# Kernel tuning notes

Measured on AMD Instinct MI355X. Metric: run time of the kernel, lower is better.

The kernel has to match this reference:

```python
import jax, jax.numpy as jnp
import numpy as np
import math

EPS = 1e-6

def _rmsnorm(x, w):
    var = jnp.mean(x * x, axis=-1, keepdims=True)
    return x * jax.lax.rsqrt(var + EPS) * w

def _rotary(x, cos, sin):
    d = x.shape[-1] // 2
    x1, x2 = x[..., :d], x[..., d:]
    return jnp.concatenate([x1 * cos - x2 * sin, x2 * cos + x1 * sin], axis=-1)

def _conv1x1(x, w):
    # x: (B, C, 1, S), w: (O, C) -> (B, O, 1, S)
    return jnp.einsum('bcls,oc->bols', x, w)

def setup_inputs() -> dict:
    key = jax.random.key(0)
    ks = jax.random.split(key, 12)
    B, H, KVH, D, S, T, HID = 8, 16, 2, 128, 16, 8192, 2048
    return {
        'x': jax.random.normal(ks[0], (B, HID, 1, S), jnp.float32),
        'cos': jax.random.uniform(ks[1], (1, 1, S, D // 2), jnp.float32),
        'sin': jax.random.uniform(ks[2], (1, 1, S, D // 2), jnp.float32),
        'kv_cache_k': jax.random.normal(ks[3], (B, KVH, T, D), jnp.float32),
        'kv_cache_v': jax.random.normal(ks[4], (B, KVH, T, D), jnp.float32),
        'position': 4096,
        'mask': jnp.zeros((1, 1, S, T), jnp.float32),
        'wq': jax.random.normal(ks[5], (H * D, HID), jnp.float32) * 0.02,
        'wk': jax.random.normal(ks[6], (KVH * D, HID), jnp.float32) * 0.02,
        'wv': jax.random.normal(ks[7], (KVH * D, HID), jnp.float32) * 0.02,
        'wo': jax.random.normal(ks[8], (HID, H * D), jnp.float32) * 0.02,
        'q_norm_w': jnp.ones((D,), jnp.float32),
        'k_norm_w': jnp.ones((D,), jnp.float32),
    }

def reference(x, cos, sin, kv_cache_k, kv_cache_v, position, mask,
              wq, wk, wv, wo, q_norm_w, k_norm_w):
    B, S = x.shape[0], x.shape[3]
    D = q_norm_w.shape[0]
    H = wq.shape[0] // D
    KVH = wk.shape[0] // D
    G = H // KVH  # GQA group size

    # projections (1x1 conv == channel matmul), then (B, h, S, D)
    q = _conv1x1(x, wq)[:, :, 0, :].reshape(B, H, D, S).transpose(0, 1, 3, 2)
    k = _conv1x1(x, wk)[:, :, 0, :].reshape(B, KVH, D, S).transpose(0, 1, 3, 2)
    v = _conv1x1(x, wv)[:, :, 0, :].reshape(B, KVH, D, S).transpose(0, 1, 3, 2)

    q = _rotary(_rmsnorm(q, q_norm_w), cos, sin)
    k = _rotary(_rmsnorm(k, k_norm_w), cos, sin)

    # scatter new k/v into cache at `position`
    new_k = jax.lax.dynamic_update_slice(kv_cache_k, k, (0, 0, position, 0))
    new_v = jax.lax.dynamic_update_slice(kv_cache_v, v, (0, 0, position, 0))

    # GQA: fold q heads into (kv_head, group) so K/V need no repeat_interleave
    scale = 1.0 / math.sqrt(D)
    qg = q.reshape(B, KVH, G, S, D)
    attn = jnp.einsum('bkgsd,bktd->bkgst', qg, new_k) * scale
    attn = attn + mask[:, :, None, :, :]  # (1,1,S,T) -> broadcast over groups
    probs = jax.nn.softmax(attn, axis=-1)
    out = jnp.einsum('bkgst,bktd->bkgsd', probs, new_v).reshape(B, H, S, D)

    # back to (B, H*D, 1, S) and output projection
    out = out.transpose(0, 1, 3, 2).reshape(B, H * D, 1, S)
    out = _conv1x1(out, wo)
    return out, new_k, new_v
```

## Files before the change

### kernel.cpp

```cpp
#include <hip/hip_runtime.h>
#include <cstdint>
#include <cstddef>


typedef __attribute__((ext_vector_type(8))) short bf16x8;
typedef __attribute__((ext_vector_type(4))) float f32x4;
typedef unsigned short u16;
typedef unsigned int u32;

#define MFMA16(a, b, c) __builtin_amdgcn_mfma_f32_16x16x32_bf16(a, b, c, 0, 0, 0)

static __device__ __forceinline__ u16 f2bf(float f) {
  u32 u = __float_as_uint(f);
  u += 0x7FFFu + ((u >> 16) & 1u);
  return (u16)(u >> 16);
}
static __device__ __forceinline__ float bf2f(u16 u) {
  return __uint_as_float(((u32)u) << 16);
}
static __device__ __forceinline__ u32 pk2(float a, float b) {
  return (u32)f2bf(a) | ((u32)f2bf(b) << 16);
}

__global__ __launch_bounds__(256) void transpose_x(const float* __restrict__ x,
                                                   u16* __restrict__ Xt) {
  int id = blockIdx.x * 256 + threadIdx.x;
  int b = id >> 13, c = (id >> 2) & 2047, s4 = id & 3;
  float4 v = *(const float4*)(x + ((size_t)(b * 2048 + c)) * 16 + s4 * 4);
  size_t base = (size_t)(b * 16 + s4 * 4) * 2048 + c;
  Xt[base]        = f2bf(v.x);
  Xt[base + 2048] = f2bf(v.y);
  Xt[base + 4096] = f2bf(v.z);
  Xt[base + 6144] = f2bf(v.w);
}

template <int MODE>
__global__ __launch_bounds__(256) void gemm16(const float* __restrict__ w0,
                                              const float* __restrict__ w1,
                                              const float* __restrict__ w2,
                                              const u16* __restrict__ Bt,
                                              float* __restrict__ outp) {
  __shared__ __align__(16) u16 sW[16 * 256];
  const int tid = threadIdx.x, lane = tid & 63, w = tid >> 6;
  const int q = lane >> 4, n = lane & 15;
  const int m0 = blockIdx.x * 16;
  const float* wbase;
  if (MODE == 0) {
    if (m0 < 2048)      wbase = w0 + (size_t)m0 * 2048;
    else if (m0 < 2304) wbase = w1 + (size_t)(m0 - 2048) * 2048;
    else                wbase = w2 + (size_t)(m0 - 2304) * 2048;
  } else {
    wbase = w0 + (size_t)m0 * 2048;
  }
  f32x4 acc0 = {0.f, 0.f, 0.f, 0.f}, acc1 = acc0;

  for (int c0 = 0; c0 < 2048; c0 += 256) {
    {
      int m = tid >> 4, s16 = tid & 15;
      const float* src = wbase + (size_t)m * 2048 + c0 + s16 * 16;
      float4 a = *(const float4*)(src);
      float4 b = *(const float4*)(src + 4);
      float4 c = *(const float4*)(src + 8);
      float4 d = *(const float4*)(src + 12);
      uint4 u0 = {pk2(a.x, a.y), pk2(a.z, a.w), pk2(b.x, b.y), pk2(b.z, b.w)};
      uint4 u1 = {pk2(c.x, c.y), pk2(c.z, c.w), pk2(d.x, d.y), pk2(d.z, d.w)};
      int G0 = 2 * s16;
      *(uint4*)&sW[m * 256 + ((G0 + m) & 31) * 8]     = u0;
      *(uint4*)&sW[m * 256 + ((G0 + 1 + m) & 31) * 8] = u1;
    }
    __syncthreads();
    bf16x8 bfr[2][8];
#pragma unroll
    for (int e = 0; e < 2; ++e) {
      int j = 32 * w + 16 * e + n;
      const u16* bp = Bt + (size_t)j * 2048 + c0 + q * 8;
#pragma unroll
      for (int ks = 0; ks < 8; ++ks) bfr[e][ks] = *(const bf16x8*)(bp + ks * 32);
    }
#pragma unroll
    for (int ks = 0; ks < 8; ++ks) {
      bf16x8 af = *(const bf16x8*)&sW[n * 256 + (((4 * ks + q) + n) & 31) * 8];
      acc0 = MFMA16(af, bfr[0][ks], acc0);
      acc1 = MFMA16(af, bfr[1][ks], acc1);
    }
    __syncthreads();
  }
#pragma unroll
  for (int e = 0; e < 2; ++e) {
    f32x4 a = e ? acc1 : acc0;
    int j = 32 * w + 16 * e + n;
#pragma unroll
    for (int reg = 0; reg < 4; ++reg) {
      int m = m0 + 4 * q + reg;
      if (MODE == 0) outp[(size_t)m * 128 + j] = a[reg];
      else outp[(size_t)(j >> 4) * 32768 + m * 16 + (j & 15)] = a[reg];
    }
  }
}

__global__ __launch_bounds__(256) void norm_rot(
    const float* __restrict__ qkv, const float* __restrict__ cosb,
    const float* __restrict__ sinb, const float* __restrict__ qw,
    const float* __restrict__ kw,
    u16* __restrict__ Qa, float* __restrict__ knew, float* __restrict__ vnew) {
  const int wid = blockIdx.x * 4 + (threadIdx.x >> 6);
  const int lane = threadIdx.x & 63;
  const float SCALE = 0.08838834764831845f;
  if (wid < 2048) {
    int b = wid >> 8, h = (wid >> 4) & 15, s = wid & 15;
    int j = b * 16 + s;
    float v1 = qkv[(size_t)(h * 128 + lane) * 128 + j];
    float v2 = qkv[(size_t)(h * 128 + lane + 64) * 128 + j];
    float ss = v1 * v1 + v2 * v2;
#pragma unroll
    for (int o = 32; o > 0; o >>= 1) ss += __shfl_xor(ss, o, 64);
    float rr = rsqrtf(ss * (1.0f / 128.0f) + 1e-6f);
    float n1 = v1 * rr * qw[lane];
    float n2 = v2 * rr * qw[lane + 64];
    float c = cosb[s * 64 + lane], sn = sinb[s * 64 + lane];
    u16* dst = Qa + (size_t)((b * 16 + h) * 16 + s) * 128;
    dst[lane]      = f2bf((n1 * c - n2 * sn) * SCALE);
    dst[lane + 64] = f2bf((n2 * c + n1 * sn) * SCALE);
  } else if (wid < 2304) {
    int idx = wid - 2048;
    int b = idx >> 5, kvh = (idx >> 4) & 1, s = idx & 15;
    int j = b * 16 + s;
    int row = 2048 + kvh * 128;
    float v1 = qkv[(size_t)(row + lane) * 128 + j];
    float v2 = qkv[(size_t)(row + lane + 64) * 128 + j];
    float ss = v1 * v1 + v2 * v2;
#pragma unroll
    for (int o = 32; o > 0; o >>= 1) ss += __shfl_xor(ss, o, 64);
    float rr = rsqrtf(ss * (1.0f / 128.0f) + 1e-6f);
    float n1 = v1 * rr * kw[lane];
    float n2 = v2 * rr * kw[lane + 64];
    float c = cosb[s * 64 + lane], sn = sinb[s * 64 + lane];
    float* dst = knew + (size_t)((b * 2 + kvh) * 16 + s) * 128;
    dst[lane]      = n1 * c - n2 * sn;
    dst[lane + 64] = n2 * c + n1 * sn;
  } else {
    int idx = wid - 2304;
    int b = idx >> 5, kvh = (idx >> 4) & 1, s = idx & 15;
    int j = b * 16 + s;
    int row = 2304 + kvh * 128;
    float* dst = vnew + (size_t)((b * 2 + kvh) * 16 + s) * 128;
    dst[lane]      = qkv[(size_t)(row + lane) * 128 + j];
    dst[lane + 64] = qkv[(size_t)(row + lane + 64) * 128 + j];
  }
}

__global__ __launch_bounds__(256, 2) void attn(
    const u16* __restrict__ Qa, const float* __restrict__ kcache,
    const float* __restrict__ vcache, const float* __restrict__ knew,
    const float* __restrict__ vnew, const int* __restrict__ posp,
    const float* __restrict__ mask, float* __restrict__ outk,
    float* __restrict__ outv, u16* __restrict__ Opart,
    float* __restrict__ Mpart, float* __restrict__ Lpart) {
  __shared__ __align__(16) u16 sQ[16384];
  __shared__ __align__(16) u16 sP[8192];
  __shared__ __align__(16) u16 sVt[8192];

  const int tid = threadIdx.x, lane = tid & 63, w = tid >> 6;
  const int q = lane >> 4, n = lane & 15;
  const int bid = blockIdx.x;
  const int bk = bid >> 5, chunk = bid & 31;
  const int b = bk >> 1, kvh = bk & 1;
  const int pos = *posp;

  for (int i = tid; i < 2048; i += 256) {
    int r = i >> 4, g = i & 15;
    int h = kvh * 8 + (r >> 4), s = r & 15;
    uint4 v = *(const uint4*)(Qa + (size_t)((b * 16 + h) * 16 + s) * 128 + g * 8);
    *(uint4*)&sQ[r * 128 + ((g + r) & 15) * 8] = v;
  }
  __syncthreads();
  bf16x8 qf[2][4];
#pragma unroll
  for (int e = 0; e < 2; ++e) {
    int r = 32 * w + 16 * e + n;
#pragma unroll
    for (int ks = 0; ks < 4; ++ks)
      qf[e][ks] = *(const bf16x8*)&sQ[r * 128 + (((4 * ks + q) + r) & 15) * 8];
  }
  __syncthreads();

  bf16x8 idE = {0, 0, 0, 0, 0, 0, 0, 0}, idO = idE;
  {
    const short one = (short)0x3F80;
    int tq = n >> 3, te = n & 7;
#pragma unroll
    for (int e = 0; e < 8; ++e) {
      if (q == tq && e == te) idE[e] = one;
      if (q == tq + 2 && e == te) idO[e] = one;
    }
  }

  float m_old[2] = {-INFINITY, -INFINITY}, l_old[2] = {0.f, 0.f};
  f32x4 oacc[2][8];
#pragma unroll
  for (int e = 0; e < 2; ++e)
#pragma unroll
    for (int nt = 0; nt < 8; ++nt) oacc[e][nt] = (f32x4){0.f, 0.f, 0.f, 0.f};

  for (int tile = 0; tile < 4; ++tile) {
    const int t0 = chunk * 256 + tile * 64;
    for (int i = tid; i < 2048; i += 256) {
      int isV = i >> 10;
      int tl = (i >> 4) & 63, g = i & 15;
      int tg = t0 + tl;
      const float* src;
      float* dst;
      if (!isV) {
        src = (tg >= pos && tg < pos + 16)
                  ? (knew + (size_t)(bk * 16 + (tg - pos)) * 128)
                  : (kcache + ((size_t)bk * 8192 + tg) * 128);
        dst = outk + ((size_t)bk * 8192 + tg) * 128;
      } else {
        src = (tg >= pos && tg < pos + 16)
                  ? (vnew + (size_t)(bk * 16 + (tg - pos)) * 128)
                  : (vcache + ((size_t)bk * 8192 + tg) * 128);
        dst = outv + ((size_t)bk * 8192 + tg) * 128;
      }
      float4 a = *(const float4*)(src + g * 8);
      float4 b2 = *(const float4*)(src + g * 8 + 4);
      *(float4*)(dst + g * 8) = a;
      *(float4*)(dst + g * 8 + 4) = b2;
      uint4 u = {pk2(a.x, a.y), pk2(a.z, a.w), pk2(b2.x, b2.y), pk2(b2.z, b2.w)};
      *(uint4*)&sQ[isV * 8192 + tl * 128 + ((g + tl) & 15) * 8] = u;
    }
    float mv[4][4];
#pragma unroll
    for (int mt = 0; mt < 4; ++mt)
#pragma unroll
      for (int rg = 0; rg < 4; ++rg)
        mv[mt][rg] = mask[(size_t)n * 8192 + t0 + 16 * mt + 4 * q + rg];
    __syncthreads();

    f32x4 sacc[4][2];
#pragma unroll
    for (int mt = 0; mt < 4; ++mt) {
      sacc[mt][0] = (f32x4){0.f, 0.f, 0.f, 0.f};
      sacc[mt][1] = sacc[mt][0];
    }
#pragma unroll
    for (int ks = 0; ks < 4; ++ks) {
#pragma unroll
      for (int mt = 0; mt < 4; ++mt) {
        int trow = 16 * mt + n;
        bf16x8 kf = *(const bf16x8*)&sQ[trow * 128 + (((4 * ks + q) + trow) & 15) * 8];
        sacc[mt][0] = MFMA16(kf, qf[0][ks], sacc[mt][0]);
        sacc[mt][1] = MFMA16(kf, qf[1][ks], sacc[mt][1]);
      }
    }

#pragma unroll
    for (int mtv = 0; mtv < 4; ++mtv) {
      int trow = 16 * mtv + n;
      bf16x8 vfr = *(const bf16x8*)&sQ[8192 + trow * 128 + (((4 * w + q) + trow) & 15) * 8];
      f32x4 z = {0.f, 0.f, 0.f, 0.f};
      f32x4 d0 = MFMA16(vfr, idE, z);
      f32x4 d1 = MFMA16(vfr, idO, z);
      int G = 2 * mtv + (q >> 1), off = 4 * (q & 1);
      int dp0 = 32 * w + n, dp1 = dp0 + 16;
      uint2 u0 = {pk2(d0[0], d0[1]), pk2(d0[2], d0[3])};
      uint2 u1 = {pk2(d1[0], d1[1]), pk2(d1[2], d1[3])};
      *(uint2*)&sVt[dp0 * 64 + ((G + dp0) & 7) * 8 + off] = u0;
      *(uint2*)&sVt[dp1 * 64 + ((G + dp1) & 7) * 8 + off] = u1;
    }

    float al[2];
#pragma unroll
    for (int e = 0; e < 2; ++e) {
      float sv[4][4];
      float mx = -INFINITY;
#pragma unroll
      for (int mt = 0; mt < 4; ++mt)
#pragma unroll
        for (int rg = 0; rg < 4; ++rg) {
          float v = sacc[mt][e][rg] + mv[mt][rg];
          sv[mt][rg] = v;
          mx = fmaxf(mx, v);
        }
      mx = fmaxf(mx, __shfl_xor(mx, 16));
      mx = fmaxf(mx, __shfl_xor(mx, 32));
      float mn = fmaxf(m_old[e], mx);
      al[e] = __expf(m_old[e] - mn);
      float ts = 0.f;
      int r = 32 * w + 16 * e + n;
#pragma unroll
      for (int mt = 0; mt < 4; ++mt) {
        float p0 = __expf(sv[mt][0] - mn), p1 = __expf(sv[mt][1] - mn);
        float p2 = __expf(sv[mt][2] - mn), p3 = __expf(sv[mt][3] - mn);
        ts += (p0 + p1) + (p2 + p3);
        uint2 up = {pk2(p0, p1), pk2(p2, p3)};
        int G = 2 * mt + (q >> 1), off = 4 * (q & 1);
        *(uint2*)&sP[r * 64 + ((G + r) & 7) * 8 + off] = up;
      }
      ts += __shfl_xor(ts, 16);
      ts += __shfl_xor(ts, 32);
      l_old[e] = l_old[e] * al[e] + ts;
      m_old[e] = mn;
    }
    __syncthreads();

#pragma unroll
    for (int e = 0; e < 2; ++e) {
      float an[4];
#pragma unroll
      for (int rg = 0; rg < 4; ++rg) an[rg] = __shfl(al[e], 4 * q + rg);
#pragma unroll
      for (int nt = 0; nt < 8; ++nt)
#pragma unroll
        for (int rg = 0; rg < 4; ++rg) oacc[e][nt][rg] *= an[rg];
    }
    bf16x8 Pf[2][2];
#pragma unroll
    for (int e = 0; e < 2; ++e) {
      int r = 32 * w + 16 * e + n;
#pragma unroll
      for (int ks = 0; ks < 2; ++ks)
        Pf[e][ks] = *(const bf16x8*)&sP[r * 64 + (((4 * ks + q) + r) & 7) * 8];
    }
#pragma unroll
    for (int nt = 0; nt < 8; ++nt) {
      int d = 16 * nt + n;
#pragma unroll
      for (int ks = 0; ks < 2; ++ks) {
        bf16x8 vf = *(const bf16x8*)&sVt[d * 64 + (((4 * ks + q) + d) & 7) * 8];
        oacc[0][nt] = MFMA16(Pf[0][ks], vf, oacc[0][nt]);
        oacc[1][nt] = MFMA16(Pf[1][ks], vf, oacc[1][nt]);
      }
    }
    __syncthreads();
  }

#pragma unroll
  for (int e = 0; e < 2; ++e)
#pragma unroll
    for (int nt = 0; nt < 8; ++nt) {
      int d = 16 * nt + n;
      int r0 = 32 * w + 16 * e + 4 * q;
      int G = r0 >> 3, off = 4 * (q & 1);
      uint2 u = {pk2(oacc[e][nt][0], oacc[e][nt][1]),
                 pk2(oacc[e][nt][2], oacc[e][nt][3])};
      *(uint2*)&sQ[d * 128 + ((G + d) & 15) * 8 + off] = u;
    }
  if (q == 0) {
#pragma unroll
    for (int e = 0; e < 2; ++e) {
      int r = 32 * w + 16 * e + n;
      Mpart[(size_t)bid * 128 + r] = m_old[e];
      Lpart[(size_t)bid * 128 + r] = l_old[e];
    }
  }
  __syncthreads();
  for (int i = tid; i < 2048; i += 256) {
    int d = i >> 4, g = i & 15;
    uint4 v = *(const uint4*)&sQ[d * 128 + ((g + d) & 15) * 8];
    *(uint4*)(Opart + (size_t)bid * 16384 + d * 128 + g * 8) = v;
  }
}

__global__ __launch_bounds__(256) void combine(const u16* __restrict__ Opart,
                                               const float* __restrict__ Mp,
                                               const float* __restrict__ Lp,
                                               u16* __restrict__ A2t) {
  __shared__ float wgt[32 * 128];
  const int tid = threadIdx.x;
  const int bk = blockIdx.x, dgrp = blockIdx.y;
  if (tid < 128) {
    int r = tid;
    float mc[32], M = -INFINITY;
#pragma unroll
    for (int c = 0; c < 32; ++c) {
      mc[c] = Mp[(size_t)(bk * 32 + c) * 128 + r];
      M = fmaxf(M, mc[c]);
    }
    float L = 0.f, wv[32];
#pragma unroll
    for (int c = 0; c < 32; ++c) {
      wv[c] = __expf(mc[c] - M);
      L += wv[c] * Lp[(size_t)(bk * 32 + c) * 128 + r];
    }
    float inv = 1.0f / L;
#pragma unroll
    for (int c = 0; c < 32; ++c) wgt[c * 128 + r] = wv[c] * inv;
  }
  __syncthreads();
  int r = tid & 127, dd = tid >> 7;
  int b = bk >> 1, kvh = bk & 1;
  int h = kvh * 8 + (r >> 4), s = r & 15;
  size_t arow = (size_t)(b * 16 + s) * 2048 + h * 128;
  for (int di = 0; di < 8; ++di) {
    int d = dgrp * 16 + dd + 2 * di;
    float o = 0.f;
#pragma unroll
    for (int c = 0; c < 32; ++c)
      o += wgt[c * 128 + r] *
           bf2f(Opart[((size_t)(bk * 32 + c) * 128 + d) * 128 + r]);
    A2t[arow + d] = f2bf(o);
  }
}

extern "C" void kernel_launch(void* const* d_in, const int* in_sizes, int n_in,
                              void* d_out, int out_size, void* d_ws, size_t ws_size,
                              hipStream_t stream) {
  const float* x    = (const float*)d_in[0];
  const float* cosb = (const float*)d_in[1];
  const float* sinb = (const float*)d_in[2];
  const float* kc   = (const float*)d_in[3];
  const float* vc   = (const float*)d_in[4];
  const int*   posp = (const int*)d_in[5];
  const float* mask = (const float*)d_in[6];
  const float* wq   = (const float*)d_in[7];
  const float* wk   = (const float*)d_in[8];
  const float* wv   = (const float*)d_in[9];
  const float* wo   = (const float*)d_in[10];
  const float* qw   = (const float*)d_in[11];
  const float* kw   = (const float*)d_in[12];

  float* out  = (float*)d_out;
  float* outk = out + 262144;
  float* outv = outk + 16777216;

  float* ws      = (float*)d_ws;
  float* ws_qkv  = ws;
  float* ws_knew = ws + 327680;
  float* ws_vnew = ws + 360448;
  u16*   ws_Qa   = (u16*)(ws + 393216);
  u16*   ws_Xt   = (u16*)(ws + 524288);
  u16*   ws_A2t  = (u16*)(ws + 655360);
  float* ws_M    = ws + 786432;
  float* ws_L    = ws + 851968;
  u16*   ws_O    = (u16*)(ws + 917504);

  transpose_x<<<256, 256, 0, stream>>>(x, ws_Xt);
  gemm16<0><<<160, 256, 0, stream>>>(wq, wk, wv, ws_Xt, ws_qkv);
  norm_rot<<<640, 256, 0, stream>>>(ws_qkv, cosb, sinb, qw, kw,
                                    ws_Qa, ws_knew, ws_vnew);
  attn<<<512, 256, 0, stream>>>(ws_Qa, kc, vc, ws_knew, ws_vnew, posp, mask,
                                outk, outv, ws_O, ws_M, ws_L);
  combine<<<dim3(16, 8), 256, 0, stream>>>(ws_O, ws_M, ws_L, ws_A2t);
  gemm16<1><<<128, 256, 0, stream>>>(wo, wo, wo, ws_A2t, out);
}
```

Measured before the change: 346.3 us.

## Prefetch KV tiles in registers, split-K GEMM blocks, transpose QKV output layout

The attention kernel now loads the next K/V tile into registers while the current tile is being computed, and it prefetches the mask. Q fragments are read straight from global memory instead of being staged through LDS. One of the per-tile barriers is dropped by merging the LDS buffers into one region. The projection GEMMs use 512-thread blocks that split K across two halves and reduce through LDS. The QKV output is stored row-major per token, so the GEMM writes and the norm_rot reads are contiguous. In exchange, register pressure in the attention kernel rises, and removing the trailing barrier needs the LDS regions to be disjoint to stay race-free.

After: 365.9 us. 1.06x slower.

```diff
diff --git a/kernel.cpp b/kernel.cpp
--- a/kernel.cpp
+++ b/kernel.cpp
@@ -35,13 +35,17 @@
 }
 
 template <int MODE>
-__global__ __launch_bounds__(256) void gemm16(const float* __restrict__ w0,
+__global__ __launch_bounds__(512) void gemm16(const float* __restrict__ w0,
                                               const float* __restrict__ w1,
                                               const float* __restrict__ w2,
                                               const u16* __restrict__ Bt,
                                               float* __restrict__ outp) {
-  __shared__ __align__(16) u16 sW[16 * 256];
-  const int tid = threadIdx.x, lane = tid & 63, w = tid >> 6;
+  __shared__ __align__(16) u16 sW[2][16 * 256];
+  __shared__ __align__(16) float sRed[2048];
+  const int t512 = threadIdx.x;
+  const int half = t512 >> 8;
+  const int tid = t512 & 255;
+  const int lane = tid & 63, w = tid >> 6;
   const int q = lane >> 4, n = lane & 15;
   const int m0 = blockIdx.x * 16;
   const float* wbase;
@@ -52,9 +56,10 @@
   } else {
     wbase = w0 + (size_t)m0 * 2048;
   }
+  const int kbase = half * 1024;
   f32x4 acc0 = {0.f, 0.f, 0.f, 0.f}, acc1 = acc0;
 
-  for (int c0 = 0; c0 < 2048; c0 += 256) {
+  for (int c0 = kbase; c0 < kbase + 1024; c0 += 256) {
     {
       int m = tid >> 4, s16 = tid & 15;
       const float* src = wbase + (size_t)m * 2048 + c0 + s16 * 16;
@@ -65,8 +70,8 @@
       uint4 u0 = {pk2(a.x, a.y), pk2(a.z, a.w), pk2(b.x, b.y), pk2(b.z, b.w)};
       uint4 u1 = {pk2(c.x, c.y), pk2(c.z, c.w), pk2(d.x, d.y), pk2(d.z, d.w)};
       int G0 = 2 * s16;
-      *(uint4*)&sW[m * 256 + ((G0 + m) & 31) * 8]     = u0;
-      *(uint4*)&sW[m * 256 + ((G0 + 1 + m) & 31) * 8] = u1;
+      *(uint4*)&sW[half][m * 256 + ((G0 + m) & 31) * 8]     = u0;
+      *(uint4*)&sW[half][m * 256 + ((G0 + 1 + m) & 31) * 8] = u1;
     }
     __syncthreads();
     bf16x8 bfr[2][8];
@@ -79,21 +84,33 @@
     }
 #pragma unroll
     for (int ks = 0; ks < 8; ++ks) {
-      bf16x8 af = *(const bf16x8*)&sW[n * 256 + (((4 * ks + q) + n) & 31) * 8];
+      bf16x8 af = *(const bf16x8*)&sW[half][n * 256 + (((4 * ks + q) + n) & 31) * 8];
       acc0 = MFMA16(af, bfr[0][ks], acc0);
       acc1 = MFMA16(af, bfr[1][ks], acc1);
     }
     __syncthreads();
   }
-#pragma unroll
-  for (int e = 0; e < 2; ++e) {
-    f32x4 a = e ? acc1 : acc0;
-    int j = 32 * w + 16 * e + n;
-#pragma unroll
-    for (int reg = 0; reg < 4; ++reg) {
-      int m = m0 + 4 * q + reg;
-      if (MODE == 0) outp[(size_t)m * 128 + j] = a[reg];
-      else outp[(size_t)(j >> 4) * 32768 + m * 16 + (j & 15)] = a[reg];
+  if (half == 1) {
+    *(f32x4*)&sRed[tid * 8]     = acc0;
+    *(f32x4*)&sRed[tid * 8 + 4] = acc1;
+  }
+  __syncthreads();
+  if (half == 0) {
+    acc0 += *(const f32x4*)&sRed[tid * 8];
+    acc1 += *(const f32x4*)&sRed[tid * 8 + 4];
+#pragma unroll
+    for (int e = 0; e < 2; ++e) {
+      f32x4 a = e ? acc1 : acc0;
+      int j = 32 * w + 16 * e + n;
+      if (MODE == 0) {
+        *(f32x4*)&outp[(size_t)j * 2560 + m0 + 4 * q] = a;
+      } else {
+#pragma unroll
+        for (int reg = 0; reg < 4; ++reg) {
+          int m = m0 + 4 * q + reg;
+          outp[(size_t)(j >> 4) * 32768 + m * 16 + (j & 15)] = a[reg];
+        }
+      }
     }
   }
 }
@@ -109,8 +126,9 @@
   if (wid < 2048) {
     int b = wid >> 8, h = (wid >> 4) & 15, s = wid & 15;
     int j = b * 16 + s;
-    float v1 = qkv[(size_t)(h * 128 + lane) * 128 + j];
-    float v2 = qkv[(size_t)(h * 128 + lane + 64) * 128 + j];
+    const float* row = qkv + (size_t)j * 2560 + h * 128;
+    float v1 = row[lane];
+    float v2 = row[lane + 64];
     float ss = v1 * v1 + v2 * v2;
 #pragma unroll
     for (int o = 32; o > 0; o >>= 1) ss += __shfl_xor(ss, o, 64);
@@ -125,9 +143,9 @@
     int idx = wid - 2048;
     int b = idx >> 5, kvh = (idx >> 4) & 1, s = idx & 15;
     int j = b * 16 + s;
-    int row = 2048 + kvh * 128;
-    float v1 = qkv[(size_t)(row + lane) * 128 + j];
-    float v2 = qkv[(size_t)(row + lane + 64) * 128 + j];
+    const float* row = qkv + (size_t)j * 2560 + 2048 + kvh * 128;
+    float v1 = row[lane];
+    float v2 = row[lane + 64];
     float ss = v1 * v1 + v2 * v2;
 #pragma unroll
     for (int o = 32; o > 0; o >>= 1) ss += __shfl_xor(ss, o, 64);
@@ -142,10 +160,10 @@
     int idx = wid - 2304;
     int b = idx >> 5, kvh = (idx >> 4) & 1, s = idx & 15;
     int j = b * 16 + s;
-    int row = 2304 + kvh * 128;
+    const float* row = qkv + (size_t)j * 2560 + 2304 + kvh * 128;
     float* dst = vnew + (size_t)((b * 2 + kvh) * 16 + s) * 128;
-    dst[lane]      = qkv[(size_t)(row + lane) * 128 + j];
-    dst[lane + 64] = qkv[(size_t)(row + lane + 64) * 128 + j];
+    dst[lane]      = row[lane];
+    dst[lane + 64] = row[lane + 64];
   }
 }
 
@@ -156,9 +174,7 @@
     const float* __restrict__ mask, float* __restrict__ outk,
     float* __restrict__ outv, u16* __restrict__ Opart,
     float* __restrict__ Mpart, float* __restrict__ Lpart) {
-  __shared__ __align__(16) u16 sQ[16384];
-  __shared__ __align__(16) u16 sP[8192];
-  __shared__ __align__(16) u16 sVt[8192];
+  __shared__ __align__(16) u16 lds[32768];
 
   const int tid = threadIdx.x, lane = tid & 63, w = tid >> 6;
   const int q = lane >> 4, n = lane & 15;
@@ -167,22 +183,54 @@
   const int b = bk >> 1, kvh = bk & 1;
   const int pos = *posp;
 
-  for (int i = tid; i < 2048; i += 256) {
-    int r = i >> 4, g = i & 15;
-    int h = kvh * 8 + (r >> 4), s = r & 15;
-    uint4 v = *(const uint4*)(Qa + (size_t)((b * 16 + h) * 16 + s) * 128 + g * 8);
-    *(uint4*)&sQ[r * 128 + ((g + r) & 15) * 8] = v;
-  }
-  __syncthreads();
+  const int stl = tid >> 4;
+  const int g = tid & 15;
+
+#define SRC_PTR(isV_, tg_)                                                   \
+  ((isV_) ? (((tg_) >= pos && (tg_) < pos + 16)                              \
+                 ? (vnew + (size_t)(bk * 16 + ((tg_) - pos)) * 128)          \
+                 : (vcache + ((size_t)bk * 8192 + (tg_)) * 128))             \
+          : (((tg_) >= pos && (tg_) < pos + 16)                              \
+                 ? (knew + (size_t)(bk * 16 + ((tg_) - pos)) * 128)          \
+                 : (kcache + ((size_t)bk * 8192 + (tg_)) * 128)))
+
+  float4 pf[8][2];
+#define ISSUE_STAGE(tile_)                                                   \
+  {                                                                          \
+    const int t0_ = chunk * 256 + (tile_) * 64;                              \
+    _Pragma("unroll") for (int u = 0; u < 8; ++u) {                          \
+      int isV_ = u >> 2;                                                     \
+      int tl_ = (stl + 16 * u) & 63;                                         \
+      int tg_ = t0_ + tl_;                                                   \
+      const float* s_ = SRC_PTR(isV_, tg_) + g * 8;                          \
+      pf[u][0] = *(const float4*)(s_);                                       \
+      pf[u][1] = *(const float4*)(s_ + 4);                                   \
+    }                                                                        \
+  }
+
+  float4 mv4[4];
+#define LOAD_MASK(tile_)                                                     \
+  {                                                                          \
+    const int t0_ = chunk * 256 + (tile_) * 64;                              \
+    _Pragma("unroll") for (int mt = 0; mt < 4; ++mt)                         \
+        mv4[mt] =                                                            \
+        *(const float4*)(mask + (size_t)n * 8192 + t0_ + 16 * mt + 4 * q);   \
+  }
+
+  ISSUE_STAGE(0);
+
   bf16x8 qf[2][4];
 #pragma unroll
   for (int e = 0; e < 2; ++e) {
     int r = 32 * w + 16 * e + n;
+    int h = kvh * 8 + (r >> 4), s = r & 15;
+    const u16* qrow = Qa + (size_t)((b * 16 + h) * 16 + s) * 128;
 #pragma unroll
     for (int ks = 0; ks < 4; ++ks)
-      qf[e][ks] = *(const bf16x8*)&sQ[r * 128 + (((4 * ks + q) + r) & 15) * 8];
-  }
-  __syncthreads();
+      qf[e][ks] = *(const bf16x8*)(qrow + (4 * ks + q) * 8);
+  }
+
+  LOAD_MASK(0);
 
   bf16x8 idE = {0, 0, 0, 0, 0, 0, 0, 0}, idO = idE;
   {
@@ -204,37 +252,21 @@
 
   for (int tile = 0; tile < 4; ++tile) {
     const int t0 = chunk * 256 + tile * 64;
-    for (int i = tid; i < 2048; i += 256) {
-      int isV = i >> 10;
-      int tl = (i >> 4) & 63, g = i & 15;
+#pragma unroll
+    for (int u = 0; u < 8; ++u) {
+      int isV = u >> 2;
+      int tl = (stl + 16 * u) & 63;
       int tg = t0 + tl;
-      const float* src;
-      float* dst;
-      if (!isV) {
-        src = (tg >= pos && tg < pos + 16)
-                  ? (knew + (size_t)(bk * 16 + (tg - pos)) * 128)
-                  : (kcache + ((size_t)bk * 8192 + tg) * 128);
-        dst = outk + ((size_t)bk * 8192 + tg) * 128;
-      } else {
-        src = (tg >= pos && tg < pos + 16)
-                  ? (vnew + (size_t)(bk * 16 + (tg - pos)) * 128)
-                  : (vcache + ((size_t)bk * 8192 + tg) * 128);
-        dst = outv + ((size_t)bk * 8192 + tg) * 128;
-      }
-      float4 a = *(const float4*)(src + g * 8);
-      float4 b2 = *(const float4*)(src + g * 8 + 4);
-      *(float4*)(dst + g * 8) = a;
-      *(float4*)(dst + g * 8 + 4) = b2;
-      uint4 u = {pk2(a.x, a.y), pk2(a.z, a.w), pk2(b2.x, b2.y), pk2(b2.z, b2.w)};
-      *(uint4*)&sQ[isV * 8192 + tl * 128 + ((g + tl) & 15) * 8] = u;
-    }
-    float mv[4][4];
-#pragma unroll
-    for (int mt = 0; mt < 4; ++mt)
-#pragma unroll
-      for (int rg = 0; rg < 4; ++rg)
-        mv[mt][rg] = mask[(size_t)n * 8192 + t0 + 16 * mt + 4 * q + rg];
+      float* dst = (isV ? outv : outk) + ((size_t)bk * 8192 + tg) * 128 + g * 8;
+      float4 a = pf[u][0], b2 = pf[u][1];
+      *(float4*)dst = a;
+      *(float4*)(dst + 4) = b2;
+      uint4 uu = {pk2(a.x, a.y), pk2(a.z, a.w), pk2(b2.x, b2.y), pk2(b2.z, b2.w)};
+      *(uint4*)&lds[isV * 8192 + tl * 128 + ((g + tl) & 15) * 8] = uu;
+    }
     __syncthreads();
+
+    if (tile < 3) { ISSUE_STAGE(tile + 1); }
 
     f32x4 sacc[4][2];
 #pragma unroll
@@ -247,7 +279,7 @@
 #pragma unroll
       for (int mt = 0; mt < 4; ++mt) {
         int trow = 16 * mt + n;
-        bf16x8 kf = *(const bf16x8*)&sQ[trow * 128 + (((4 * ks + q) + trow) & 15) * 8];
+        bf16x8 kf = *(const bf16x8*)&lds[trow * 128 + (((4 * ks + q) + trow) & 15) * 8];
         sacc[mt][0] = MFMA16(kf, qf[0][ks], sacc[mt][0]);
         sacc[mt][1] = MFMA16(kf, qf[1][ks], sacc[mt][1]);
       }
@@ -256,7 +288,7 @@
 #pragma unroll
     for (int mtv = 0; mtv < 4; ++mtv) {
       int trow = 16 * mtv + n;
-      bf16x8 vfr = *(const bf16x8*)&sQ[8192 + trow * 128 + (((4 * w + q) + trow) & 15) * 8];
+      bf16x8 vfr = *(const bf16x8*)&lds[8192 + trow * 128 + (((4 * w + q) + trow) & 15) * 8];
       f32x4 z = {0.f, 0.f, 0.f, 0.f};
       f32x4 d0 = MFMA16(vfr, idE, z);
       f32x4 d1 = MFMA16(vfr, idO, z);
@@ -264,8 +296,8 @@
       int dp0 = 32 * w + n, dp1 = dp0 + 16;
       uint2 u0 = {pk2(d0[0], d0[1]), pk2(d0[2], d0[3])};
       uint2 u1 = {pk2(d1[0], d1[1]), pk2(d1[2], d1[3])};
-      *(uint2*)&sVt[dp0 * 64 + ((G + dp0) & 7) * 8 + off] = u0;
-      *(uint2*)&sVt[dp1 * 64 + ((G + dp1) & 7) * 8 + off] = u1;
+      *(uint2*)&lds[24576 + dp0 * 64 + ((G + dp0) & 7) * 8 + off] = u0;
+      *(uint2*)&lds[24576 + dp1 * 64 + ((G + dp1) & 7) * 8 + off] = u1;
     }
 
     float al[2];
@@ -277,7 +309,7 @@
       for (int mt = 0; mt < 4; ++mt)
 #pragma unroll
         for (int rg = 0; rg < 4; ++rg) {
-          float v = sacc[mt][e][rg] + mv[mt][rg];
+          float v = sacc[mt][e][rg] + mv4[mt][rg];
           sv[mt][rg] = v;
           mx = fmaxf(mx, v);
         }
@@ -294,13 +326,14 @@
         ts += (p0 + p1) + (p2 + p3);
         uint2 up = {pk2(p0, p1), pk2(p2, p3)};
         int G = 2 * mt + (q >> 1), off = 4 * (q & 1);
-        *(uint2*)&sP[r * 64 + ((G + r) & 7) * 8 + off] = up;
+        *(uint2*)&lds[16384 + r * 64 + ((G + r) & 7) * 8 + off] = up;
       }
       ts += __shfl_xor(ts, 16);
       ts += __shfl_xor(ts, 32);
       l_old[e] = l_old[e] * al[e] + ts;
       m_old[e] = mn;
     }
+    if (tile < 3) { LOAD_MASK(tile + 1); }
     __syncthreads();
 
 #pragma unroll
@@ -319,19 +352,18 @@
       int r = 32 * w + 16 * e + n;
 #pragma unroll
       for (int ks = 0; ks < 2; ++ks)
-        Pf[e][ks] = *(const bf16x8*)&sP[r * 64 + (((4 * ks + q) + r) & 7) * 8];
+        Pf[e][ks] = *(const bf16x8*)&lds[16384 + r * 64 + (((4 * ks + q) + r) & 7) * 8];
     }
 #pragma unroll
     for (int nt = 0; nt < 8; ++nt) {
       int d = 16 * nt + n;
 #pragma unroll
       for (int ks = 0; ks < 2; ++ks) {
-        bf16x8 vf = *(const bf16x8*)&sVt[d * 64 + (((4 * ks + q) + d) & 7) * 8];
+        bf16x8 vf = *(const bf16x8*)&lds[24576 + d * 64 + (((4 * ks + q) + d) & 7) * 8];
         oacc[0][nt] = MFMA16(Pf[0][ks], vf, oacc[0][nt]);
         oacc[1][nt] = MFMA16(Pf[1][ks], vf, oacc[1][nt]);
       }
     }
-    __syncthreads();
   }
 
 #pragma unroll
@@ -343,7 +375,7 @@
       int G = r0 >> 3, off = 4 * (q & 1);
       uint2 u = {pk2(oacc[e][nt][0], oacc[e][nt][1]),
                  pk2(oacc[e][nt][2], oacc[e][nt][3])};
-      *(uint2*)&sQ[d * 128 + ((G + d) & 15) * 8 + off] = u;
+      *(uint2*)&lds[d * 128 + ((G + d) & 15) * 8 + off] = u;
     }
   if (q == 0) {
 #pragma unroll
@@ -355,10 +387,13 @@
   }
   __syncthreads();
   for (int i = tid; i < 2048; i += 256) {
-    int d = i >> 4, g = i & 15;
-    uint4 v = *(const uint4*)&sQ[d * 128 + ((g + d) & 15) * 8];
-    *(uint4*)(Opart + (size_t)bid * 16384 + d * 128 + g * 8) = v;
-  }
+    int d2 = i >> 4, g2 = i & 15;
+    uint4 v = *(const uint4*)&lds[d2 * 128 + ((g2 + d2) & 15) * 8];
+    *(uint4*)(Opart + (size_t)bid * 16384 + d2 * 128 + g2 * 8) = v;
+  }
+#undef SRC_PTR
+#undef ISSUE_STAGE
+#undef LOAD_MASK
 }
 
 __global__ __launch_bounds__(256) void combine(const u16* __restrict__ Opart,
@@ -435,11 +470,11 @@
   u16*   ws_O    = (u16*)(ws + 917504);
 
   transpose_x<<<256, 256, 0, stream>>>(x, ws_Xt);
-  gemm16<0><<<160, 256, 0, stream>>>(wq, wk, wv, ws_Xt, ws_qkv);
+  gemm16<0><<<160, 512, 0, stream>>>(wq, wk, wv, ws_Xt, ws_qkv);
   norm_rot<<<640, 256, 0, stream>>>(ws_qkv, cosb, sinb, qw, kw,
                                     ws_Qa, ws_knew, ws_vnew);
   attn<<<512, 256, 0, stream>>>(ws_Qa, kc, vc, ws_knew, ws_vnew, posp, mask,
                                 outk, outv, ws_O, ws_M, ws_L);
   combine<<<dim3(16, 8), 256, 0, stream>>>(ws_O, ws_M, ws_L, ws_A2t);
-  gemm16<1><<<128, 256, 0, stream>>>(wo, wo, wo, ws_A2t, out);
-}
+  gemm16<1><<<128, 512, 0, stream>>>(wo, wo, wo, ws_A2t, out);
+}
```

## Split-K the projection GEMMs across 8 partitions and widen combine grid

Applied to the files above, without the earlier changes.

Both projection GEMMs now split the 2048-long reduction into 8 slices along a second grid dimension, so each block does a single K-tile instead of looping eight times. Partial sums go to a workspace buffer and are summed either inside norm_rot (for QKV) or in a new reduce_out kernel (for the output projection). The combine kernel's grid is doubled and each thread accumulates 4 output dims at once. This raises parallelism on small, latency-bound GEMMs that previously launched only 128-160 blocks. The cost is extra partial-sum traffic, one more launch, and workspace reuse across stages.

Measured after the change: 332.4 us. -4.0%, faster.

```diff
diff --git a/kernel.cpp b/kernel.cpp
--- a/kernel.cpp
+++ b/kernel.cpp
@@ -44,6 +44,8 @@
   const int tid = threadIdx.x, lane = tid & 63, w = tid >> 6;
   const int q = lane >> 4, n = lane & 15;
   const int m0 = blockIdx.x * 16;
+  const int kp = blockIdx.y;
+  const int kbase = kp * 256;
   const float* wbase;
   if (MODE == 0) {
     if (m0 < 2048)      wbase = w0 + (size_t)m0 * 2048;
@@ -52,54 +54,64 @@
   } else {
     wbase = w0 + (size_t)m0 * 2048;
   }
+  {
+    int m = tid >> 4, s16 = tid & 15;
+    const float* src = wbase + (size_t)m * 2048 + kbase + s16 * 16;
+    float4 a = *(const float4*)(src);
+    float4 b = *(const float4*)(src + 4);
+    float4 c = *(const float4*)(src + 8);
+    float4 d = *(const float4*)(src + 12);
+    uint4 u0 = {pk2(a.x, a.y), pk2(a.z, a.w), pk2(b.x, b.y), pk2(b.z, b.w)};
+    uint4 u1 = {pk2(c.x, c.y), pk2(c.z, c.w), pk2(d.x, d.y), pk2(d.z, d.w)};
+    int G0 = 2 * s16;
+    *(uint4*)&sW[m * 256 + ((G0 + m) & 31) * 8]     = u0;
+    *(uint4*)&sW[m * 256 + ((G0 + 1 + m) & 31) * 8] = u1;
+  }
+  bf16x8 bfr[2][8];
+#pragma unroll
+  for (int e = 0; e < 2; ++e) {
+    int j = 32 * w + 16 * e + n;
+    const u16* bp = Bt + (size_t)j * 2048 + kbase + q * 8;
+#pragma unroll
+    for (int ks = 0; ks < 8; ++ks) bfr[e][ks] = *(const bf16x8*)(bp + ks * 32);
+  }
+  __syncthreads();
   f32x4 acc0 = {0.f, 0.f, 0.f, 0.f}, acc1 = acc0;
-
-  for (int c0 = 0; c0 < 2048; c0 += 256) {
-    {
-      int m = tid >> 4, s16 = tid & 15;
-      const float* src = wbase + (size_t)m * 2048 + c0 + s16 * 16;
-      float4 a = *(const float4*)(src);
-      float4 b = *(const float4*)(src + 4);
-      float4 c = *(const float4*)(src + 8);
-      float4 d = *(const float4*)(src + 12);
-      uint4 u0 = {pk2(a.x, a.y), pk2(a.z, a.w), pk2(b.x, b.y), pk2(b.z, b.w)};
-      uint4 u1 = {pk2(c.x, c.y), pk2(c.z, c.w), pk2(d.x, d.y), pk2(d.z, d.w)};
-      int G0 = 2 * s16;
-      *(uint4*)&sW[m * 256 + ((G0 + m) & 31) * 8]     = u0;
-      *(uint4*)&sW[m * 256 + ((G0 + 1 + m) & 31) * 8] = u1;
-    }
-    __syncthreads();
-    bf16x8 bfr[2][8];
-#pragma unroll
-    for (int e = 0; e < 2; ++e) {
-      int j = 32 * w + 16 * e + n;
-      const u16* bp = Bt + (size_t)j * 2048 + c0 + q * 8;
-#pragma unroll
-      for (int ks = 0; ks < 8; ++ks) bfr[e][ks] = *(const bf16x8*)(bp + ks * 32);
-    }
-#pragma unroll
-    for (int ks = 0; ks < 8; ++ks) {
-      bf16x8 af = *(const bf16x8*)&sW[n * 256 + (((4 * ks + q) + n) & 31) * 8];
-      acc0 = MFMA16(af, bfr[0][ks], acc0);
-      acc1 = MFMA16(af, bfr[1][ks], acc1);
-    }
-    __syncthreads();
+#pragma unroll
+  for (int ks = 0; ks < 8; ++ks) {
+    bf16x8 af = *(const bf16x8*)&sW[n * 256 + (((4 * ks + q) + n) & 31) * 8];
+    acc0 = MFMA16(af, bfr[0][ks], acc0);
+    acc1 = MFMA16(af, bfr[1][ks], acc1);
   }
 #pragma unroll
   for (int e = 0; e < 2; ++e) {
     f32x4 a = e ? acc1 : acc0;
     int j = 32 * w + 16 * e + n;
-#pragma unroll
-    for (int reg = 0; reg < 4; ++reg) {
-      int m = m0 + 4 * q + reg;
-      if (MODE == 0) outp[(size_t)m * 128 + j] = a[reg];
-      else outp[(size_t)(j >> 4) * 32768 + m * 16 + (j & 15)] = a[reg];
-    }
-  }
+    if (MODE == 0) {
+      *(f32x4*)&outp[(size_t)kp * 327680 + (size_t)j * 2560 + m0 + 4 * q] = a;
+    } else {
+#pragma unroll
+      for (int reg = 0; reg < 4; ++reg) {
+        int m = m0 + 4 * q + reg;
+        outp[(size_t)kp * 262144 + (size_t)(j >> 4) * 32768 + m * 16 + (j & 15)] =
+            a[reg];
+      }
+    }
+  }
+}
+
+__global__ __launch_bounds__(256) void reduce_out(const float* __restrict__ part,
+                                                  float* __restrict__ out) {
+  int i = blockIdx.x * 256 + threadIdx.x;
+  f32x4 acc = {0.f, 0.f, 0.f, 0.f};
+#pragma unroll
+  for (int p = 0; p < 8; ++p)
+    acc += *(const f32x4*)(part + (size_t)p * 262144 + (size_t)i * 4);
+  *(f32x4*)(out + (size_t)i * 4) = acc;
 }
 
 __global__ __launch_bounds__(256) void norm_rot(
-    const float* __restrict__ qkv, const float* __restrict__ cosb,
+    const float* __restrict__ qkvp, const float* __restrict__ cosb,
     const float* __restrict__ sinb, const float* __restrict__ qw,
     const float* __restrict__ kw,
     u16* __restrict__ Qa, float* __restrict__ knew, float* __restrict__ vnew) {
@@ -109,8 +121,13 @@
   if (wid < 2048) {
     int b = wid >> 8, h = (wid >> 4) & 15, s = wid & 15;
     int j = b * 16 + s;
-    float v1 = qkv[(size_t)(h * 128 + lane) * 128 + j];
-    float v2 = qkv[(size_t)(h * 128 + lane + 64) * 128 + j];
+    const float* row = qkvp + (size_t)j * 2560 + h * 128;
+    float v1 = 0.f, v2 = 0.f;
+#pragma unroll
+    for (int p = 0; p < 8; ++p) {
+      v1 += row[(size_t)p * 327680 + lane];
+      v2 += row[(size_t)p * 327680 + lane + 64];
+    }
     float ss = v1 * v1 + v2 * v2;
 #pragma unroll
     for (int o = 32; o > 0; o >>= 1) ss += __shfl_xor(ss, o, 64);
@@ -125,9 +142,13 @@
     int idx = wid - 2048;
     int b = idx >> 5, kvh = (idx >> 4) & 1, s = idx & 15;
     int j = b * 16 + s;
-    int row = 2048 + kvh * 128;
-    float v1 = qkv[(size_t)(row + lane) * 128 + j];
-    float v2 = qkv[(size_t)(row + lane + 64) * 128 + j];
+    const float* row = qkvp + (size_t)j * 2560 + 2048 + kvh * 128;
+    float v1 = 0.f, v2 = 0.f;
+#pragma unroll
+    for (int p = 0; p < 8; ++p) {
+      v1 += row[(size_t)p * 327680 + lane];
+      v2 += row[(size_t)p * 327680 + lane + 64];
+    }
     float ss = v1 * v1 + v2 * v2;
 #pragma unroll
     for (int o = 32; o > 0; o >>= 1) ss += __shfl_xor(ss, o, 64);
@@ -142,10 +163,16 @@
     int idx = wid - 2304;
     int b = idx >> 5, kvh = (idx >> 4) & 1, s = idx & 15;
     int j = b * 16 + s;
-    int row = 2304 + kvh * 128;
+    const float* row = qkvp + (size_t)j * 2560 + 2304 + kvh * 128;
+    float v1 = 0.f, v2 = 0.f;
+#pragma unroll
+    for (int p = 0; p < 8; ++p) {
+      v1 += row[(size_t)p * 327680 + lane];
+      v2 += row[(size_t)p * 327680 + lane + 64];
+    }
     float* dst = vnew + (size_t)((b * 2 + kvh) * 16 + s) * 128;
-    dst[lane]      = qkv[(size_t)(row + lane) * 128 + j];
-    dst[lane + 64] = qkv[(size_t)(row + lane + 64) * 128 + j];
+    dst[lane]      = v1;
+    dst[lane + 64] = v2;
   }
 }
 
@@ -391,14 +418,21 @@
   int b = bk >> 1, kvh = bk & 1;
   int h = kvh * 8 + (r >> 4), s = r & 15;
   size_t arow = (size_t)(b * 16 + s) * 2048 + h * 128;
-  for (int di = 0; di < 8; ++di) {
-    int d = dgrp * 16 + dd + 2 * di;
-    float o = 0.f;
-#pragma unroll
-    for (int c = 0; c < 32; ++c)
-      o += wgt[c * 128 + r] *
-           bf2f(Opart[((size_t)(bk * 32 + c) * 128 + d) * 128 + r]);
-    A2t[arow + d] = f2bf(o);
+  float o[4] = {0.f, 0.f, 0.f, 0.f};
+#pragma unroll
+  for (int c = 0; c < 32; ++c) {
+    float wv = wgt[c * 128 + r];
+    size_t base = ((size_t)(bk * 32 + c) * 128) * 128 + r;
+#pragma unroll
+    for (int di = 0; di < 4; ++di) {
+      int d = dgrp * 8 + dd + 2 * di;
+      o[di] += wv * bf2f(Opart[base + (size_t)d * 128]);
+    }
+  }
+#pragma unroll
+  for (int di = 0; di < 4; ++di) {
+    int d = dgrp * 8 + dd + 2 * di;
+    A2t[arow + d] = f2bf(o[di]);
   }
 }
 
@@ -423,23 +457,27 @@
   float* outk = out + 262144;
   float* outv = outk + 16777216;
 
-  float* ws      = (float*)d_ws;
-  float* ws_qkv  = ws;
-  float* ws_knew = ws + 327680;
-  float* ws_vnew = ws + 360448;
-  u16*   ws_Qa   = (u16*)(ws + 393216);
-  u16*   ws_Xt   = (u16*)(ws + 524288);
-  u16*   ws_A2t  = (u16*)(ws + 655360);
-  float* ws_M    = ws + 786432;
-  float* ws_L    = ws + 851968;
-  u16*   ws_O    = (u16*)(ws + 917504);
+  float* ws     = (float*)d_ws;
+  float* ws_A   = ws;
+  float* ws_knew = ws + 4194304;
+  float* ws_vnew = ws + 4227072;
+  u16*   ws_Qa   = (u16*)(ws + 4259840);
+  u16*   ws_Xt   = (u16*)(ws + 4390912);
+  u16*   ws_A2t  = (u16*)(ws + 4521984);
+  float* ws_M    = ws + 4653056;
+  float* ws_L    = ws + 4718592;
+
+  float* ws_qkvp = ws_A;
+  u16*   ws_O    = (u16*)ws_A;
+  float* ws_op   = ws_A;
 
   transpose_x<<<256, 256, 0, stream>>>(x, ws_Xt);
-  gemm16<0><<<160, 256, 0, stream>>>(wq, wk, wv, ws_Xt, ws_qkv);
-  norm_rot<<<640, 256, 0, stream>>>(ws_qkv, cosb, sinb, qw, kw,
+  gemm16<0><<<dim3(160, 8), 256, 0, stream>>>(wq, wk, wv, ws_Xt, ws_qkvp);
+  norm_rot<<<640, 256, 0, stream>>>(ws_qkvp, cosb, sinb, qw, kw,
                                     ws_Qa, ws_knew, ws_vnew);
   attn<<<512, 256, 0, stream>>>(ws_Qa, kc, vc, ws_knew, ws_vnew, posp, mask,
                                 outk, outv, ws_O, ws_M, ws_L);
-  combine<<<dim3(16, 8), 256, 0, stream>>>(ws_O, ws_M, ws_L, ws_A2t);
-  gemm16<1><<<128, 256, 0, stream>>>(wo, wo, wo, ws_A2t, out);
-}
+  combine<<<dim3(16, 16), 256, 0, stream>>>(ws_O, ws_M, ws_L, ws_A2t);
+  gemm16<1><<<dim3(128, 8), 256, 0, stream>>>(wo, wo, wo, ws_A2t, ws_op);
+  reduce_out<<<256, 256, 0, stream>>>(ws_op, out);
+}
```
